# Kernel tuning notes

Measured on AMD Instinct MI355X. Metric: run time of the kernel, lower is better.

Reference implementation:

```python
import jax, jax.numpy as jnp
import numpy as np

NKV = 8      # n_head_kv
G = 8        # n_head // n_head_kv
D = 64       # head_dim (hardcoded in source views)
NH = NKV * G # n_head = 64


def rotate_half(x):
    x1, x2 = x[..., : D // 2], x[..., D // 2:]
    return jnp.concatenate((-x2, x1), axis=-1)


def setup_inputs() -> dict:
    key = jax.random.key(0)
    ks = jax.random.split(key, 9)
    B, S, H = 2, 1024, 4096
    hidden_states = jax.random.normal(ks[0], (B, S, H), dtype=jnp.float32)
    alibi = jnp.zeros((B * NH, 1, S), dtype=jnp.float32)            # unused in this forward path
    attention_mask = jnp.zeros((B, 1, S, S), dtype=jnp.float32)      # unused (is_causal=True)
    cos = jax.random.uniform(ks[1], (S, D), dtype=jnp.float32, minval=-1.0, maxval=1.0)
    sin = jax.random.uniform(ks[2], (S, D), dtype=jnp.float32, minval=-1.0, maxval=1.0)
    wq = jax.random.normal(ks[3], (H, H), dtype=jnp.float32) * 0.02          # Linear weight (out, in)
    wk = jax.random.normal(ks[4], (NKV * D, H), dtype=jnp.float32) * 0.02
    wv = jax.random.normal(ks[5], (NKV * D, H), dtype=jnp.float32) * 0.02
    wd = jax.random.normal(ks[6], (H, H), dtype=jnp.float32) * 0.02          # dense weight
    return {"hidden_states": hidden_states, "alibi": alibi, "attention_mask": attention_mask,
            "cos": cos, "sin": sin, "wq": wq, "wk": wk, "wv": wv, "wd": wd}


def reference(hidden_states, alibi, attention_mask, cos, sin, wq, wk, wv, wd):
    B, S, H = hidden_states.shape
    # fused-style projections (Linear: x @ W.T, no bias)
    # q: [B, S, NKV, G, D] -> [B, NKV, G, S, D]; head h = kv_group*G + j (group-major, matches source rearrange)
    q = (hidden_states @ wq.T).reshape(B, S, NKV, G, D).transpose(0, 2, 3, 1, 4)
    k = (hidden_states @ wk.T).reshape(B, S, NKV, D).transpose(0, 2, 1, 3)   # [B, NKV, S, D]
    v = (hidden_states @ wv.T).reshape(B, S, NKV, D).transpose(0, 2, 1, 3)
    # RoPE (cos/sin broadcast over batch/head dims)
    q = q * cos + rotate_half(q) * sin
    k = k * cos + rotate_half(k) * sin
    # grouped-query attention without materializing broadcast K/V
    inv_norm = jnp.asarray(1.0 / np.sqrt(D), dtype=hidden_states.dtype)
    scores = jnp.einsum('bkgsd,bktd->bkgst', q, k) * inv_norm        # [B, NKV, G, S, S]
    causal = jnp.tril(jnp.ones((S, S), dtype=bool))
    neg = jnp.finfo(scores.dtype).min
    scores = jnp.where(causal, scores, scores + neg)
    probs = jax.nn.softmax(scores, axis=-1)
    out = jnp.einsum('bkgst,bktd->bkgsd', probs, v)                  # [B, NKV, G, S, D]
    out = out.reshape(B, NH, S, D).transpose(0, 2, 1, 3).reshape(B, S, NH * D)
    return out @ wd.T
```

## Files before the change

kernel.cpp:

```cpp
#include <hip/hip_runtime.h>
#include <hip/hip_bf16.h>
#include <cstdint>

typedef short short8 __attribute__((ext_vector_type(8)));
typedef __bf16 bf16x8 __attribute__((ext_vector_type(8)));
typedef float float4v __attribute__((ext_vector_type(4)));
typedef float float16v __attribute__((ext_vector_type(16)));

#define NKV 8
#define G 8
#define D 64
#define NH 64
#define BB 2
#define S 1024
#define H 4096
#define MROWS (BB*S)
#define NQKV (H + 2*NKV*D)

__device__ __forceinline__ unsigned short f2b(float f) {
    union { float f; uint32_t u; } v; v.f = f;
    uint32_t u = v.u;
    uint32_t r = (u + 0x7FFFu + ((u >> 16) & 1u)) >> 16;
    return (unsigned short)r;
}
__device__ __forceinline__ float b2f(unsigned short b) {
    union { float f; uint32_t u; } v; v.u = ((uint32_t)b) << 16;
    return v.f;
}

__device__ __forceinline__ void gload_lds16(const unsigned short* g, unsigned short* l) {
    __builtin_amdgcn_global_load_lds(
        (const __attribute__((address_space(1))) uint32_t*)g,
        (__attribute__((address_space(3))) uint32_t*)l, 16, 0, 0);
}

__global__ void cvt_all(const float* __restrict__ hs, const float* __restrict__ wq,
                        const float* __restrict__ wk, const float* __restrict__ wv,
                        const float* __restrict__ wd,
                        unsigned short* __restrict__ hs_b, unsigned short* __restrict__ wqkv_b,
                        unsigned short* __restrict__ wd_b) {
    const size_t N0 = (size_t)MROWS * H;
    const size_t N1 = (size_t)H * H;
    const size_t N2 = (size_t)512 * H;
    const size_t N3 = (size_t)512 * H;
    const size_t N4 = (size_t)H * H;
    const size_t total4 = (N0 + N1 + N2 + N3 + N4) / 4;
    size_t i = (size_t)blockIdx.x * blockDim.x + threadIdx.x;
    const size_t stride = (size_t)gridDim.x * blockDim.x;
    for (; i < total4; i += stride) {
        size_t e = i * 4;
        const float* s; unsigned short* d;
        if (e < N0)                { s = hs + e;                  d = hs_b + e; }
        else if (e < N0+N1)        { s = wq + (e-N0);             d = wqkv_b + (e-N0); }
        else if (e < N0+N1+N2)     { s = wk + (e-N0-N1);          d = wqkv_b + N1 + (e-N0-N1); }
        else if (e < N0+N1+N2+N3)  { s = wv + (e-N0-N1-N2);       d = wqkv_b + N1+N2 + (e-N0-N1-N2); }
        else                       { s = wd + (e-N0-N1-N2-N3);    d = wd_b + (e-N0-N1-N2-N3); }
        float4 f = *(const float4*)s;
        ushort4 o;
        o.x = f2b(f.x); o.y = f2b(f.y); o.z = f2b(f.z); o.w = f2b(f.w);
        *(ushort4*)d = o;
    }
}

template <bool BF16_OUT>
__global__ __launch_bounds__(256) void gemm_nt(
    const unsigned short* __restrict__ A, const unsigned short* __restrict__ W,
    void* __restrict__ Cv, int M, int N, int K) {
    __shared__ unsigned short As[128 * 32];
    __shared__ unsigned short Bs[128 * 32];
    const int bm = blockIdx.y * 128, bn = blockIdx.x * 128;
    const int tid = threadIdx.x;
    const int w = tid >> 6, lane = tid & 63;
    const int n32 = lane & 31, khalf = lane >> 5;
    const int wm = (w & 1) * 64, wn = (w >> 1) * 64;

    const int r0 = tid >> 2;
    const int c0 = (tid & 3) ^ ((r0 >> 2) & 3);
    const unsigned short* pA0 = A + (size_t)(bm + r0) * K + c0 * 8;
    const unsigned short* pA1 = A + (size_t)(bm + r0 + 64) * K + c0 * 8;
    const unsigned short* pW0 = W + (size_t)(bn + r0) * K + c0 * 8;
    const unsigned short* pW1 = W + (size_t)(bn + r0 + 64) * K + c0 * 8;
    unsigned short* Asl0 = As + tid * 8;
    unsigned short* Asl1 = As + 2048 + tid * 8;
    unsigned short* Bsl0 = Bs + tid * 8;
    unsigned short* Bsl1 = Bs + 2048 + tid * 8;

    const unsigned short* aP[2][2];
    const unsigned short* bP[2][2];
#pragma unroll
    for (int g = 0; g < 2; g++)
#pragma unroll
        for (int s = 0; s < 2; s++) {
            int cp = ((s << 1) | khalf) ^ ((n32 >> 2) & 3);
            aP[g][s] = &As[(wm + g * 32 + n32) * 32 + cp * 8];
            bP[g][s] = &Bs[(wn + g * 32 + n32) * 32 + cp * 8];
        }

    float16v acc[2][2] = {};

    const int iters = K >> 5;
    for (int it = 0; it < iters; ++it) {
        __syncthreads();
        gload_lds16(pA0, Asl0);
        gload_lds16(pA1, Asl1);
        gload_lds16(pW0, Bsl0);
        gload_lds16(pW1, Bsl1);
        pA0 += 32; pA1 += 32; pW0 += 32; pW1 += 32;
        __syncthreads();
        bf16x8 af[2][2], bf[2][2];
#pragma unroll
        for (int g = 0; g < 2; g++)
#pragma unroll
            for (int s = 0; s < 2; s++) {
                af[g][s] = *(const bf16x8*)aP[g][s];
                bf[g][s] = *(const bf16x8*)bP[g][s];
            }
#pragma unroll
        for (int s = 0; s < 2; s++)
#pragma unroll
            for (int mg = 0; mg < 2; mg++)
#pragma unroll
                for (int ng = 0; ng < 2; ng++)
                    acc[mg][ng] = __builtin_amdgcn_mfma_f32_32x32x16_bf16(
                        af[mg][s], bf[ng][s], acc[mg][ng], 0, 0, 0);
    }

#pragma unroll
    for (int mg = 0; mg < 2; mg++) {
#pragma unroll
        for (int ng = 0; ng < 2; ng++) {
            int gcol = bn + wn + ng * 32 + n32;
#pragma unroll
            for (int reg = 0; reg < 16; reg++) {
                int grow = bm + wm + mg * 32 + (reg & 3) + 8 * (reg >> 2) + 4 * khalf;
                if (BF16_OUT)
                    ((unsigned short*)Cv)[(size_t)grow * N + gcol] = f2b(acc[mg][ng][reg]);
                else
                    ((float*)Cv)[(size_t)grow * N + gcol] = acc[mg][ng][reg];
            }
        }
    }
}

__global__ void rope_scatter(const unsigned short* __restrict__ qkv,
                             const float* __restrict__ cosb, const float* __restrict__ sinb,
                             unsigned short* __restrict__ qa, unsigned short* __restrict__ ka,
                             unsigned short* __restrict__ vt) {
    int idx = blockIdx.x * blockDim.x + threadIdx.x;
    const int total = MROWS * NQKV;
    const int stride = gridDim.x * blockDim.x;
    for (; idx < total; idx += stride) {
        int row = idx / NQKV, o = idx - row * NQKV;
        int b = row >> 10, s = row & 1023;
        float x = b2f(qkv[idx]);
        if (o < H) {
            int kv = o >> 9, g = (o >> 6) & 7, d = o & 63;
            int po = (d < 32) ? idx + 32 : idx - 32;
            float partner = b2f(qkv[po]);
            float rot = (d < 32) ? -partner : partner;
            float y = x * cosb[s * 64 + d] + rot * sinb[s * 64 + d];
            int h = b * 64 + kv * 8 + g;
            qa[(size_t)h * (S * D) + s * 64 + d] = f2b(y);
        } else if (o < H + 512) {
            int o2 = o - H;
            int kv = o2 >> 6, d = o2 & 63;
            int po = (d < 32) ? idx + 32 : idx - 32;
            float partner = b2f(qkv[po]);
            float rot = (d < 32) ? -partner : partner;
            float y = x * cosb[s * 64 + d] + rot * sinb[s * 64 + d];
            ka[(size_t)(b * NKV + kv) * (S * D) + s * 64 + d] = f2b(y);
        } else {
            int o2 = o - H - 512;
            int kv = o2 >> 6, d = o2 & 63;
            vt[(size_t)(b * NKV + kv) * (D * S) + (size_t)d * S + s] = qkv[idx];
        }
    }
}

__global__ __launch_bounds__(256) void attn_kernel(
    const unsigned short* __restrict__ qa, const unsigned short* __restrict__ ka,
    const unsigned short* __restrict__ vt, unsigned short* __restrict__ out) {
    __shared__ unsigned short Ks[64 * 72];
    __shared__ unsigned short Vs[64 * 72];
    __shared__ unsigned short Ps[4 * 16 * 72];
    const int p = blockIdx.x;
    const int yy = blockIdx.y;
    const int b = yy >> 5, kvh = (yy >> 2) & 7, gp = yy & 3;
    const int h0 = b * 64 + kvh * 8 + gp * 2;
    const int tid = threadIdx.x, w = tid >> 6, lane = tid & 63;
    const int col = lane & 15, quad = lane >> 4;
    const unsigned short* Kg = ka + (size_t)(b * NKV + kvh) * (S * D);
    const unsigned short* Vg = vt + (size_t)(b * NKV + kvh) * (D * S);
    const int srow = tid >> 3, scc = (tid & 7) * 8;
    float4v zero4 = {0.f, 0.f, 0.f, 0.f};
    const float SC2 = 0.125f * 1.44269504089f;

#pragma unroll
    for (int part = 0; part < 2; part++) {
        const int qt = part ? (15 - p) : p;
        const int qb = qt * 64;

        bf16x8 aq[2][2];
#pragma unroll
        for (int hd = 0; hd < 2; hd++)
#pragma unroll
            for (int c = 0; c < 2; c++)
                aq[hd][c] = *(const bf16x8*)&qa[(size_t)(h0 + hd) * (S * D) + (size_t)qb * D
                                               + (w * 16 + col) * 64 + c * 32 + quad * 8];

        float m_run[2][4], l_run[2][4];
        float4v o_acc[2][4];
#pragma unroll
        for (int hd = 0; hd < 2; hd++) {
#pragma unroll
            for (int r = 0; r < 4; r++) { m_run[hd][r] = -1e30f; l_run[hd][r] = 0.f; }
#pragma unroll
            for (int dg = 0; dg < 4; dg++) o_acc[hd][dg] = zero4;
        }

        for (int kt = 0; kt <= qt; kt++) {
            const int kb = kt * 64;
            __syncthreads();
            *(short8*)&Ks[srow * 72 + scc]        = *(const short8*)&Kg[(kb + srow) * 64 + scc];
            *(short8*)&Ks[(srow + 32) * 72 + scc] = *(const short8*)&Kg[(kb + srow + 32) * 64 + scc];
            *(short8*)&Vs[srow * 72 + scc]        = *(const short8*)&Vg[(size_t)srow * S + kb + scc];
            *(short8*)&Vs[(srow + 32) * 72 + scc] = *(const short8*)&Vg[(size_t)(srow + 32) * S + kb + scc];
            __syncthreads();

#pragma unroll
            for (int hd = 0; hd < 2; hd++) {
                float4v sc[4];
#pragma unroll
                for (int n16 = 0; n16 < 4; n16++) {
                    bf16x8 bk0 = *(const bf16x8*)&Ks[(n16 * 16 + col) * 72 + quad * 8];
                    bf16x8 bk1 = *(const bf16x8*)&Ks[(n16 * 16 + col) * 72 + 32 + quad * 8];
                    float4v a = __builtin_amdgcn_mfma_f32_16x16x32_bf16(aq[hd][0], bk0, zero4, 0, 0, 0);
                    sc[n16] = __builtin_amdgcn_mfma_f32_16x16x32_bf16(aq[hd][1], bk1, a, 0, 0, 0);
                }
#pragma unroll
                for (int n16 = 0; n16 < 4; n16++) {
                    int key = kb + n16 * 16 + col;
#pragma unroll
                    for (int r = 0; r < 4; r++) {
                        int qrow = qb + w * 16 + quad * 4 + r;
                        float sv = sc[n16][r] * SC2;
                        sc[n16][r] = (key <= qrow) ? sv : -1e30f;
                    }
                }
#pragma unroll
                for (int r = 0; r < 4; r++) {
                    float mx = fmaxf(fmaxf(sc[0][r], sc[1][r]), fmaxf(sc[2][r], sc[3][r]));
#pragma unroll
                    for (int off = 1; off < 16; off <<= 1) mx = fmaxf(mx, __shfl_xor(mx, off));
                    float mnew = fmaxf(m_run[hd][r], mx);
                    float alpha = __builtin_amdgcn_exp2f(m_run[hd][r] - mnew);
                    float rsum = 0.f;
#pragma unroll
                    for (int n16 = 0; n16 < 4; n16++) {
                        float pr = __builtin_amdgcn_exp2f(sc[n16][r] - mnew);
                        sc[n16][r] = pr;
                        rsum += pr;
                    }
#pragma unroll
                    for (int off = 1; off < 16; off <<= 1) rsum += __shfl_xor(rsum, off);
                    l_run[hd][r] = l_run[hd][r] * alpha + rsum;
                    m_run[hd][r] = mnew;
#pragma unroll
                    for (int dg = 0; dg < 4; dg++) o_acc[hd][dg][r] *= alpha;
                }
#pragma unroll
                for (int n16 = 0; n16 < 4; n16++)
#pragma unroll
                    for (int r = 0; r < 4; r++)
                        Ps[w * 1152 + (quad * 4 + r) * 72 + n16 * 16 + col] = f2b(sc[n16][r]);
                bf16x8 ap[2];
#pragma unroll
                for (int c = 0; c < 2; c++)
                    ap[c] = *(const bf16x8*)&Ps[w * 1152 + col * 72 + c * 32 + quad * 8];
#pragma unroll
                for (int dg = 0; dg < 4; dg++) {
                    bf16x8 bv0 = *(const bf16x8*)&Vs[(dg * 16 + col) * 72 + quad * 8];
                    bf16x8 bv1 = *(const bf16x8*)&Vs[(dg * 16 + col) * 72 + 32 + quad * 8];
                    float4v t = __builtin_amdgcn_mfma_f32_16x16x32_bf16(ap[0], bv0, o_acc[hd][dg], 0, 0, 0);
                    o_acc[hd][dg] = __builtin_amdgcn_mfma_f32_16x16x32_bf16(ap[1], bv1, t, 0, 0, 0);
                }
            }
        }
#pragma unroll
        for (int hd = 0; hd < 2; hd++) {
            const int hcol = ((h0 + hd) & 63) * 64;
#pragma unroll
            for (int r = 0; r < 4; r++) {
                float inv = 1.f / l_run[hd][r];
                int grow = b * S + qb + w * 16 + quad * 4 + r;
#pragma unroll
                for (int dg = 0; dg < 4; dg++)
                    out[(size_t)grow * H + hcol + dg * 16 + col] = f2b(o_acc[hd][dg][r] * inv);
            }
        }
    }
}

extern "C" void kernel_launch(void* const* d_in, const int* in_sizes, int n_in,
                              void* d_out, int out_size, void* d_ws, size_t ws_size,
                              hipStream_t stream) {
    const float* hs   = (const float*)d_in[0];
    const float* cosb = (const float*)d_in[3];
    const float* sinb = (const float*)d_in[4];
    const float* wq   = (const float*)d_in[5];
    const float* wk   = (const float*)d_in[6];
    const float* wv   = (const float*)d_in[7];
    const float* wd   = (const float*)d_in[8];

    char* p = (char*)d_ws;
    auto alloc = [&](size_t bytes) { char* r = p; p += (bytes + 255) & ~(size_t)255; return r; };
    unsigned short* wqkv_b = (unsigned short*)alloc((size_t)NQKV * H * 2);
    unsigned short* wd_b   = (unsigned short*)alloc((size_t)H * H * 2);
    unsigned short* qkv    = (unsigned short*)alloc((size_t)MROWS * NQKV * 2);
    unsigned short* qa     = (unsigned short*)alloc((size_t)BB * NH * S * D * 2);
    unsigned short* ka     = (unsigned short*)alloc((size_t)BB * NKV * S * D * 2);
    unsigned short* vt     = (unsigned short*)alloc((size_t)BB * NKV * S * D * 2);
    unsigned short* hs_b   = (unsigned short*)alloc((size_t)MROWS * H * 2);
    unsigned short* ao     = hs_b;

    cvt_all<<<4096, 256, 0, stream>>>(hs, wq, wk, wv, wd, hs_b, wqkv_b, wd_b);

    gemm_nt<true><<<dim3(NQKV / 128, MROWS / 128), 256, 0, stream>>>(hs_b, wqkv_b, qkv, MROWS, NQKV, H);
    rope_scatter<<<4096, 256, 0, stream>>>(qkv, cosb, sinb, qa, ka, vt);
    attn_kernel<<<dim3(8, 64), 256, 0, stream>>>(qa, ka, vt, ao);
    gemm_nt<false><<<dim3(H / 128, MROWS / 128), 256, 0, stream>>>(ao, wd_b, d_out, MROWS, H, H);
}
```

Baseline: 504.0 us.

## Replace GEMMs with 256x256 double-buffered 8-wave pipelined kernel and split-K

Both projection GEMMs now use a new 512-thread kernel with 256x256 tiles, 64-wide K steps, double-buffered LDS with interleaved global-to-LDS loads and MFMA 16x16x32 phases, explicit waitcnt/barrier scheduling, setprio, and an XCD-aware block swizzle. The output projection uses split-K of 2 with atomic float adds into a zeroed output, which keeps more workgroups busy since 256x256 tiles give few blocks. The aim is to hide memory latency and raise MFMA utilisation over the old single-buffered 128x128 kernel. In exchange the output depends on atomic ordering, an extra memset runs, and correctness relies on K being divisible by the tile pipeline.

New measurement: 517.2 us. 2.6% more time.

```diff
diff --git a/kernel.cpp b/kernel.cpp
--- a/kernel.cpp
+++ b/kernel.cpp
@@ -62,81 +62,112 @@
     }
 }
 
-template <bool BF16_OUT>
-__global__ __launch_bounds__(256) void gemm_nt(
+#define STAGE_A(BUF, HH, T) { \
+    const unsigned short* s_ = Ab + (size_t)((HH) * 128) * K + (T) * 64; \
+    unsigned short* d_ = &smem[(BUF) * 32768 + (HH) * 8192 + dst0]; \
+    gload_lds16(s_, d_); \
+    gload_lds16(s_ + (size_t)64 * K, d_ + 4096); }
+#define STAGE_B(BUF, HH, T) { \
+    const unsigned short* s_ = Wb + (size_t)((HH) * 128) * K + (T) * 64; \
+    unsigned short* d_ = &smem[(BUF) * 32768 + 16384 + (HH) * 8192 + dst0]; \
+    gload_lds16(s_, d_); \
+    gload_lds16(s_ + (size_t)64 * K, d_ + 4096); }
+#define RD_A4(BUF, MOFF) { \
+    _Pragma("unroll") \
+    for (int m_ = 0; m_ < 4; m_++) { \
+      af[m_][0] = *(const bf16x8*)&smem[(BUF) * 32768 + arow0 + ((MOFF) + m_) * 1024 + sl0]; \
+      af[m_][1] = *(const bf16x8*)&smem[(BUF) * 32768 + arow0 + ((MOFF) + m_) * 1024 + sl1]; } }
+#define RD_B8(BUF) { \
+    _Pragma("unroll") \
+    for (int n_ = 0; n_ < 4; n_++) { \
+      bf[n_][0] = *(const bf16x8*)&smem[(BUF) * 32768 + brow0 + n_ * 1024 + sl0]; \
+      bf[n_][1] = *(const bf16x8*)&smem[(BUF) * 32768 + brow0 + n_ * 1024 + sl1]; } }
+#define PTAIL() { __builtin_amdgcn_s_barrier(); \
+    asm volatile("s_waitcnt lgkmcnt(0)" ::: "memory"); \
+    __builtin_amdgcn_sched_barrier(0); }
+#define QUAD(MB, NB) { __builtin_amdgcn_s_setprio(1); \
+    _Pragma("unroll") \
+    for (int s_ = 0; s_ < 2; s_++) \
+    _Pragma("unroll") \
+    for (int m_ = 0; m_ < 4; m_++) \
+    _Pragma("unroll") \
+    for (int n_ = 0; n_ < 2; n_++) \
+      acc[(MB) + m_][(NB) + n_] = __builtin_amdgcn_mfma_f32_16x16x32_bf16( \
+          af[m_][s_], bf[(NB) + n_][s_], acc[(MB) + m_][(NB) + n_], 0, 0, 0); \
+    __builtin_amdgcn_s_setprio(0); }
+#define EBAR() __builtin_amdgcn_s_barrier();
+#define VM6() asm volatile("s_waitcnt vmcnt(6)" ::: "memory");
+
+template <int OUT_MODE>
+__global__ __launch_bounds__(512) void gemm8p(
     const unsigned short* __restrict__ A, const unsigned short* __restrict__ W,
-    void* __restrict__ Cv, int M, int N, int K) {
-    __shared__ unsigned short As[128 * 32];
-    __shared__ unsigned short Bs[128 * 32];
-    const int bm = blockIdx.y * 128, bn = blockIdx.x * 128;
+    void* __restrict__ Cv, int M, int N, int K, int ksplit) {
+    __shared__ unsigned short smem[65536];
     const int tid = threadIdx.x;
-    const int w = tid >> 6, lane = tid & 63;
-    const int n32 = lane & 31, khalf = lane >> 5;
-    const int wm = (w & 1) * 64, wn = (w >> 1) * 64;
-
-    const int r0 = tid >> 2;
-    const int c0 = (tid & 3) ^ ((r0 >> 2) & 3);
-    const unsigned short* pA0 = A + (size_t)(bm + r0) * K + c0 * 8;
-    const unsigned short* pA1 = A + (size_t)(bm + r0 + 64) * K + c0 * 8;
-    const unsigned short* pW0 = W + (size_t)(bn + r0) * K + c0 * 8;
-    const unsigned short* pW1 = W + (size_t)(bn + r0 + 64) * K + c0 * 8;
-    unsigned short* Asl0 = As + tid * 8;
-    unsigned short* Asl1 = As + 2048 + tid * 8;
-    unsigned short* Bsl0 = Bs + tid * 8;
-    unsigned short* Bsl1 = Bs + 2048 + tid * 8;
-
-    const unsigned short* aP[2][2];
-    const unsigned short* bP[2][2];
-#pragma unroll
-    for (int g = 0; g < 2; g++)
-#pragma unroll
-        for (int s = 0; s < 2; s++) {
-            int cp = ((s << 1) | khalf) ^ ((n32 >> 2) & 3);
-            aP[g][s] = &As[(wm + g * 32 + n32) * 32 + cp * 8];
-            bP[g][s] = &Bs[(wn + g * 32 + n32) * 32 + cp * 8];
-        }
-
-    float16v acc[2][2] = {};
-
-    const int iters = K >> 5;
-    for (int it = 0; it < iters; ++it) {
-        __syncthreads();
-        gload_lds16(pA0, Asl0);
-        gload_lds16(pA1, Asl1);
-        gload_lds16(pW0, Bsl0);
-        gload_lds16(pW1, Bsl1);
-        pA0 += 32; pA1 += 32; pW0 += 32; pW1 += 32;
-        __syncthreads();
-        bf16x8 af[2][2], bf[2][2];
-#pragma unroll
-        for (int g = 0; g < 2; g++)
-#pragma unroll
-            for (int s = 0; s < 2; s++) {
-                af[g][s] = *(const bf16x8*)aP[g][s];
-                bf[g][s] = *(const bf16x8*)bP[g][s];
-            }
-#pragma unroll
-        for (int s = 0; s < 2; s++)
-#pragma unroll
-            for (int mg = 0; mg < 2; mg++)
-#pragma unroll
-                for (int ng = 0; ng < 2; ng++)
-                    acc[mg][ng] = __builtin_amdgcn_mfma_f32_32x32x16_bf16(
-                        af[mg][s], bf[ng][s], acc[mg][ng], 0, 0, 0);
-    }
-
-#pragma unroll
-    for (int mg = 0; mg < 2; mg++) {
-#pragma unroll
-        for (int ng = 0; ng < 2; ng++) {
-            int gcol = bn + wn + ng * 32 + n32;
-#pragma unroll
-            for (int reg = 0; reg < 16; reg++) {
-                int grow = bm + wm + mg * 32 + (reg & 3) + 8 * (reg >> 2) + 4 * khalf;
-                if (BF16_OUT)
-                    ((unsigned short*)Cv)[(size_t)grow * N + gcol] = f2b(acc[mg][ng][reg]);
+    const int lane = tid & 63;
+    const int w = tid >> 6;
+    const int wm = w >> 2, wn = w & 3;
+    const int col16 = lane & 15, quad = lane >> 4;
+
+    const int gx = gridDim.x, gy = gridDim.y;
+    const int nwg = gx * gy * gridDim.z;
+    const int orig = blockIdx.x + gx * (blockIdx.y + gy * blockIdx.z);
+    const int swzb = (orig & 7) * (nwg >> 3) + (orig >> 3);
+    const int bx = swzb % gx;
+    const int rem = swzb / gx;
+    const int by = rem % gy, bz = rem / gy;
+    const int bm = by << 8, bn = bx << 8;
+    const int Kloc = K / ksplit;
+    const int k0 = bz * Kloc;
+    const int nt = Kloc >> 6;
+    const int niter = nt >> 1;
+
+    const int srow = tid >> 3;
+    const int csw8 = ((tid & 7) ^ (srow & 7)) * 8;
+    const unsigned short* Ab = A + (size_t)(bm + srow) * K + k0 + csw8;
+    const unsigned short* Wb = W + (size_t)(bn + srow) * K + k0 + csw8;
+    const int dst0 = srow * 64 + (tid & 7) * 8;
+
+    const int xk = col16 & 7;
+    const int sl0 = (quad ^ xk) * 8;
+    const int sl1 = ((quad + 4) ^ xk) * 8;
+    const int arow0 = (wm * 128 + col16) * 64;
+    const int brow0 = (wn * 64 + col16) * 64 + 16384;
+
+    float4v acc[8][4] = {};
+    bf16x8 af[4][2], bf[4][2];
+
+    STAGE_B(0, 0, 0) STAGE_B(0, 1, 0) STAGE_A(0, 0, 0) STAGE_A(0, 1, 0)
+    STAGE_B(1, 0, 1) STAGE_B(1, 1, 1) STAGE_A(1, 0, 1)
+    asm volatile("s_waitcnt vmcnt(6)" ::: "memory");
+    __builtin_amdgcn_s_barrier();
+
+    for (int i = 0; i < niter; ++i) {
+        const int t = i * 2;
+        const int tc2 = (t + 2 < nt) ? t + 2 : nt - 1;
+        const int tc3 = (t + 3 < nt) ? t + 3 : nt - 1;
+        RD_A4(0, 0) RD_B8(0) STAGE_A(1, 1, t + 1) PTAIL() QUAD(0, 0) EBAR()
+        STAGE_B(0, 0, tc2)                        PTAIL() QUAD(0, 2) EBAR()
+        RD_A4(0, 4)          STAGE_B(0, 1, tc2)   PTAIL() QUAD(4, 2) EBAR()
+        STAGE_A(0, 0, tc2)                        PTAIL() QUAD(4, 0) VM6() EBAR()
+        RD_A4(1, 0) RD_B8(1) STAGE_A(0, 1, tc2)   PTAIL() QUAD(0, 0) EBAR()
+        STAGE_B(1, 0, tc3)                        PTAIL() QUAD(0, 2) EBAR()
+        RD_A4(1, 4)          STAGE_B(1, 1, tc3)   PTAIL() QUAD(4, 2) EBAR()
+        STAGE_A(1, 0, tc3)                        PTAIL() QUAD(4, 0) VM6() EBAR()
+    }
+
+#pragma unroll
+    for (int mf = 0; mf < 8; mf++) {
+        const int gr0 = bm + wm * 128 + mf * 16 + quad * 4;
+#pragma unroll
+        for (int nf = 0; nf < 4; nf++) {
+            const int gc = bn + wn * 64 + nf * 16 + col16;
+#pragma unroll
+            for (int r = 0; r < 4; r++) {
+                if (OUT_MODE == 0)
+                    ((unsigned short*)Cv)[(size_t)(gr0 + r) * N + gc] = f2b(acc[mf][nf][r]);
                 else
-                    ((float*)Cv)[(size_t)grow * N + gcol] = acc[mg][ng][reg];
+                    unsafeAtomicAdd(&((float*)Cv)[(size_t)(gr0 + r) * N + gc], acc[mf][nf][r]);
             }
         }
     }
@@ -323,10 +354,14 @@
     unsigned short* hs_b   = (unsigned short*)alloc((size_t)MROWS * H * 2);
     unsigned short* ao     = hs_b;
 
+    hipMemsetAsync(d_out, 0, (size_t)MROWS * H * sizeof(float), stream);
+
     cvt_all<<<4096, 256, 0, stream>>>(hs, wq, wk, wv, wd, hs_b, wqkv_b, wd_b);
 
-    gemm_nt<true><<<dim3(NQKV / 128, MROWS / 128), 256, 0, stream>>>(hs_b, wqkv_b, qkv, MROWS, NQKV, H);
+    gemm8p<0><<<dim3(NQKV / 256, MROWS / 256, 1), 512, 0, stream>>>(
+        hs_b, wqkv_b, qkv, MROWS, NQKV, H, 1);
     rope_scatter<<<4096, 256, 0, stream>>>(qkv, cosb, sinb, qa, ka, vt);
     attn_kernel<<<dim3(8, 64), 256, 0, stream>>>(qa, ka, vt, ao);
-    gemm_nt<false><<<dim3(H / 128, MROWS / 128), 256, 0, stream>>>(ao, wd_b, d_out, MROWS, H, H);
-}
+    gemm8p<1><<<dim3(H / 256, MROWS / 256, 2), 512, 0, stream>>>(
+        ao, wd_b, d_out, MROWS, H, H, 2);
+}
```

## Load K/V fragments directly from global into registers, drop LDS staging and barriers

Applied to the files above, without the earlier changes.

The attention kernel no longer stages K and V tiles through shared memory with two block barriers per key tile. Each wave loads its MFMA operand fragments for K and V straight from global memory (L2-cached) into registers. MFMA sections are also wrapped with s_setprio to raise wave priority. This removes the LDS round-trip and the block synchronization, but each of the 4 waves now fetches the same K/V data redundantly, which increases global/L2 traffic and register pressure.

Result: faster. 486.3 us (-3.5%).

```diff
diff --git a/kernel.cpp b/kernel.cpp
--- a/kernel.cpp
+++ b/kernel.cpp
@@ -180,8 +180,6 @@
 __global__ __launch_bounds__(256) void attn_kernel(
     const unsigned short* __restrict__ qa, const unsigned short* __restrict__ ka,
     const unsigned short* __restrict__ vt, unsigned short* __restrict__ out) {
-    __shared__ unsigned short Ks[64 * 72];
-    __shared__ unsigned short Vs[64 * 72];
     __shared__ unsigned short Ps[4 * 16 * 72];
     const int p = blockIdx.x;
     const int yy = blockIdx.y;
@@ -191,7 +189,6 @@
     const int col = lane & 15, quad = lane >> 4;
     const unsigned short* Kg = ka + (size_t)(b * NKV + kvh) * (S * D);
     const unsigned short* Vg = vt + (size_t)(b * NKV + kvh) * (D * S);
-    const int srow = tid >> 3, scc = (tid & 7) * 8;
     float4v zero4 = {0.f, 0.f, 0.f, 0.f};
     const float SC2 = 0.125f * 1.44269504089f;
 
@@ -220,23 +217,30 @@
 
         for (int kt = 0; kt <= qt; kt++) {
             const int kb = kt * 64;
-            __syncthreads();
-            *(short8*)&Ks[srow * 72 + scc]        = *(const short8*)&Kg[(kb + srow) * 64 + scc];
-            *(short8*)&Ks[(srow + 32) * 72 + scc] = *(const short8*)&Kg[(kb + srow + 32) * 64 + scc];
-            *(short8*)&Vs[srow * 72 + scc]        = *(const short8*)&Vg[(size_t)srow * S + kb + scc];
-            *(short8*)&Vs[(srow + 32) * 72 + scc] = *(const short8*)&Vg[(size_t)(srow + 32) * S + kb + scc];
-            __syncthreads();
+            bf16x8 bk[4][2], bv[4][2];
+#pragma unroll
+            for (int n16 = 0; n16 < 4; n16++) {
+                const unsigned short* kr = &Kg[(size_t)(kb + n16 * 16 + col) * 64 + quad * 8];
+                bk[n16][0] = *(const bf16x8*)kr;
+                bk[n16][1] = *(const bf16x8*)(kr + 32);
+            }
+#pragma unroll
+            for (int dg = 0; dg < 4; dg++) {
+                const unsigned short* vr = &Vg[(size_t)(dg * 16 + col) * S + kb + quad * 8];
+                bv[dg][0] = *(const bf16x8*)vr;
+                bv[dg][1] = *(const bf16x8*)(vr + 32);
+            }
 
 #pragma unroll
             for (int hd = 0; hd < 2; hd++) {
                 float4v sc[4];
+                __builtin_amdgcn_s_setprio(1);
 #pragma unroll
                 for (int n16 = 0; n16 < 4; n16++) {
-                    bf16x8 bk0 = *(const bf16x8*)&Ks[(n16 * 16 + col) * 72 + quad * 8];
-                    bf16x8 bk1 = *(const bf16x8*)&Ks[(n16 * 16 + col) * 72 + 32 + quad * 8];
-                    float4v a = __builtin_amdgcn_mfma_f32_16x16x32_bf16(aq[hd][0], bk0, zero4, 0, 0, 0);
-                    sc[n16] = __builtin_amdgcn_mfma_f32_16x16x32_bf16(aq[hd][1], bk1, a, 0, 0, 0);
+                    float4v a = __builtin_amdgcn_mfma_f32_16x16x32_bf16(aq[hd][0], bk[n16][0], zero4, 0, 0, 0);
+                    sc[n16] = __builtin_amdgcn_mfma_f32_16x16x32_bf16(aq[hd][1], bk[n16][1], a, 0, 0, 0);
                 }
+                __builtin_amdgcn_s_setprio(0);
 #pragma unroll
                 for (int n16 = 0; n16 < 4; n16++) {
                     int key = kb + n16 * 16 + col;
@@ -277,13 +281,13 @@
 #pragma unroll
                 for (int c = 0; c < 2; c++)
                     ap[c] = *(const bf16x8*)&Ps[w * 1152 + col * 72 + c * 32 + quad * 8];
+                __builtin_amdgcn_s_setprio(1);
 #pragma unroll
                 for (int dg = 0; dg < 4; dg++) {
-                    bf16x8 bv0 = *(const bf16x8*)&Vs[(dg * 16 + col) * 72 + quad * 8];
-                    bf16x8 bv1 = *(const bf16x8*)&Vs[(dg * 16 + col) * 72 + 32 + quad * 8];
-                    float4v t = __builtin_amdgcn_mfma_f32_16x16x32_bf16(ap[0], bv0, o_acc[hd][dg], 0, 0, 0);
-                    o_acc[hd][dg] = __builtin_amdgcn_mfma_f32_16x16x32_bf16(ap[1], bv1, t, 0, 0, 0);
+                    float4v t = __builtin_amdgcn_mfma_f32_16x16x32_bf16(ap[0], bv[dg][0], o_acc[hd][dg], 0, 0, 0);
+                    o_acc[hd][dg] = __builtin_amdgcn_mfma_f32_16x16x32_bf16(ap[1], bv[dg][1], t, 0, 0, 0);
                 }
+                __builtin_amdgcn_s_setprio(0);
             }
         }
 #pragma unroll
```
